# Kernel optimization log

Hardware: AMD Instinct MI355X
Metric: run time of the kernel (lower is better)

The kernel has to match this reference:

```python
import jax, jax.numpy as jnp
import numpy as np

B, H, W, D = 16, 14, 14, 512   # map_dim D == attention_dim A (required by broadcast add)
L, HID, A = 32, 512, 512


def setup_inputs() -> dict:
    key = jax.random.key(0)
    ks = jax.random.split(key, 8)
    s = 0.02
    return {
        "maps": jax.random.normal(ks[0], (B, H, W, D), jnp.float32),
        "hiddens": jax.random.normal(ks[1], (B, L, HID), jnp.float32),
        "W_hidden": jax.random.normal(ks[2], (A, HID), jnp.float32) * s,
        "b_hidden": jnp.zeros((A,), jnp.float32),
        "W_rect": jax.random.normal(ks[3], (1, A), jnp.float32) * s,
        "b_rect": jnp.zeros((1,), jnp.float32),
        "W_co": jax.random.normal(ks[4], (HID, D), jnp.float32) * s,
        "b_co": jnp.zeros((HID,), jnp.float32),
    }


def reference(maps, hiddens, W_hidden, b_hidden, W_rect, b_rect, W_co, b_co):
    b, h, w, d = maps.shape
    fmaps = maps.reshape(b, h * w, d)                       # (B, P, D)
    hlin = hiddens @ W_hidden.T + b_hidden                  # (B, L, A)
    # additive co-attention score: ReLU(fmaps + hlin) -> linear to scalar
    rect = jax.nn.relu(fmaps[:, None, :, :] + hlin[:, :, None, :])  # (B, L, P, A)
    scores = jnp.einsum('blpa,a->blp', rect, W_rect[0]) + b_rect[0]  # (B, L, P)
    attn = jax.nn.softmax(scores, axis=2)                   # softmax over pixels P
    ctx = jnp.einsum('blp,bpd->bld', attn, fmaps)           # (B, L, D)
    co_att = (ctx @ W_co.T + b_co) * hiddens                # (B, L, HID)
    return co_att, attn
```

## Files before the change

### kernel.cpp

```cpp
#include <hip/hip_runtime.h>
#include <math.h>


typedef __attribute__((ext_vector_type(8))) short short8;
typedef __attribute__((ext_vector_type(4))) float f32x4;

__device__ __forceinline__ unsigned f2bf_u(float x) {
    union { float f; unsigned u; } c; c.f = x;
    return (c.u + 0x7FFFu + ((c.u >> 16) & 1u)) >> 16;
}
__device__ __forceinline__ unsigned pack2(float lo, float hi) {
    return f2bf_u(lo) | (f2bf_u(hi) << 16);
}
__device__ __forceinline__ uint4 pack8(const float4 a, const float4 b) {
    uint4 r;
    r.x = pack2(a.x, a.y); r.y = pack2(a.z, a.w);
    r.z = pack2(b.x, b.y); r.w = pack2(b.z, b.w);
    return r;
}

__device__ __forceinline__ void wait16(int* flags, int base) {
    if (threadIdx.x < 16) {
        while (__hip_atomic_fetch_add(&flags[(base + threadIdx.x) * 16], 0,
                                      __ATOMIC_RELAXED, __HIP_MEMORY_SCOPE_AGENT) < 1)
            __builtin_amdgcn_s_sleep(8);
    }
    __syncthreads();
    __builtin_amdgcn_fence(__ATOMIC_ACQUIRE, "agent");
}

__device__ __forceinline__ void signal1(int* flags, int idx) {
    __syncthreads();
    if (threadIdx.x == 0)
        __hip_atomic_store(&flags[idx * 16], 1, __ATOMIC_RELEASE, __HIP_MEMORY_SCOPE_AGENT);
}

template<int MODE>
__device__ __forceinline__ void gemm_body(
    const float* __restrict__ Af, const unsigned short* __restrict__ Ab,
    const float* __restrict__ Bf, const float* __restrict__ bias,
    const float* __restrict__ hmul, float* __restrict__ C,
    char* smem, int m0, int n0)
{
    uint4* As = (uint4*)smem;
    uint4* Bs = (uint4*)(smem + 32768);
    float* red = (float*)smem;
    const int tid = threadIdx.x;

    #pragma unroll
    for (int j = 0; j < 8; ++j) {
        const int S = tid + 256 * j;
        const int i = S >> 6, ln = S & 63;
        const int row  = (i & 1) * 16 + (ln & 15);
        const int col8 = (i >> 1) * 4 + (ln >> 4);
        uint4 av;
        if (MODE == 0) {
            const float* ap = Af + (size_t)(m0 + row) * 512 + col8 * 8;
            av = pack8(*(const float4*)ap, *(const float4*)(ap + 4));
        } else {
            av = *(const uint4*)(Ab + (size_t)(m0 + row) * 512 + col8 * 8);
        }
        const float* bp = Bf + (size_t)(n0 + row) * 512 + col8 * 8;
        As[S] = av;
        Bs[S] = pack8(*(const float4*)bp, *(const float4*)(bp + 4));
    }
    __syncthreads();

    const int w = tid >> 6, ln = tid & 63;
    f32x4 acc[4];
    #pragma unroll
    for (int fo = 0; fo < 4; ++fo) acc[fo] = (f32x4){0.f,0.f,0.f,0.f};
    #pragma unroll
    for (int sl = 0; sl < 4; ++sl) {
        const int s = 4 * w + sl;
        const short8 a0 = *(const short8*)&As[(2*s+0)*64 + ln];
        const short8 a1 = *(const short8*)&As[(2*s+1)*64 + ln];
        const short8 b0 = *(const short8*)&Bs[(2*s+0)*64 + ln];
        const short8 b1 = *(const short8*)&Bs[(2*s+1)*64 + ln];
        acc[0] = __builtin_amdgcn_mfma_f32_16x16x32_bf16(a0, b0, acc[0], 0, 0, 0);
        acc[1] = __builtin_amdgcn_mfma_f32_16x16x32_bf16(a0, b1, acc[1], 0, 0, 0);
        acc[2] = __builtin_amdgcn_mfma_f32_16x16x32_bf16(a1, b0, acc[2], 0, 0, 0);
        acc[3] = __builtin_amdgcn_mfma_f32_16x16x32_bf16(a1, b1, acc[3], 0, 0, 0);
    }
    __syncthreads();
    #pragma unroll
    for (int fo = 0; fo < 4; ++fo)
        #pragma unroll
        for (int r = 0; r < 4; ++r)
            red[w*1024 + fo*256 + r*64 + ln] = acc[fo][r];
    __syncthreads();
    #pragma unroll
    for (int j = 0; j < 4; ++j) {
        const int o = tid + 256 * j;
        float v = red[o] + red[1024 + o] + red[2048 + o] + red[3072 + o];
        const int fo = o >> 8, r = (o >> 6) & 3, l2 = o & 63;
        const int m = m0 + (fo >> 1) * 16 + ((l2 >> 4) << 2) + r;
        const int n = n0 + (fo & 1) * 16 + (l2 & 15);
        v += bias[n];
        if (MODE == 1) v *= hmul[(size_t)m * 512 + n];
        C[(size_t)m * 512 + n] = v;
    }
}

__device__ __forceinline__ void mid_body(
    const float* __restrict__ maps, const float* __restrict__ hlin,
    const float* __restrict__ W_rect, const float* __restrict__ b_rect,
    float* __restrict__ attn_out, unsigned int* __restrict__ ctx_out,
    char* smem, int b, int s)
{
    float* h0    = (float*)smem;
    float* h1    = h0 + 512;
    float* wv    = h0 + 1024;
    float* ftile = h0 + 1536;
    float* sraw  = ftile + 16 * 516;
    float* ep    = sraw + 2 * 208;
    float* bc    = ep + 32;

    const int l0 = 2 * s;
    const int tid = threadIdx.x;
    const int pi = tid >> 4, k = tid & 15;

    {
        const float4* H0 = (const float4*)(hlin + ((size_t)b * 32 + l0) * 512);
        const float4* H1 = (const float4*)(hlin + ((size_t)b * 32 + l0 + 1) * 512);
        const float4* WV = (const float4*)W_rect;
        if (tid < 128) { ((float4*)h0)[tid] = H0[tid]; ((float4*)wv)[tid] = WV[tid]; }
        else           { ((float4*)h1)[tid - 128] = H1[tid - 128]; }
    }
    __syncthreads();

    int aoff[8];
    float4 h0r[8], h1r[8], wr[8];
    #pragma unroll
    for (int j = 0; j < 8; ++j) {
        aoff[j] = k * 32 + ((j + k) & 7) * 4;
        h0r[j] = *(const float4*)&h0[aoff[j]];
        h1r[j] = *(const float4*)&h1[aoff[j]];
        wr[j]  = *(const float4*)&wv[aoff[j]];
    }

    const float* mb = maps + (size_t)b * 196 * 512;
    const float br = b_rect[0];
    const int d0 = tid * 2;

    float m0 = -INFINITY, m1 = -INFINITY, ls0 = 0.f, ls1 = 0.f;
    float cA0 = 0.f, cA1 = 0.f, cB0 = 0.f, cB1 = 0.f;

    for (int c = 0; c < 13; ++c) {
        __syncthreads();
        #pragma unroll
        for (int it = 0; it < 8; ++it) {
            const int idx = tid + 256 * it;
            const int r = idx >> 7, c4 = idx & 127;
            int p = c * 16 + r; if (p > 195) p = 195;
            *(float4*)&ftile[r * 516 + c4 * 4] = *(const float4*)(mb + (size_t)p * 512 + c4 * 4);
        }
        __syncthreads();

        float s0 = 0.f, s1 = 0.f;
        #pragma unroll
        for (int j = 0; j < 8; ++j) {
            const float4 f = *(const float4*)&ftile[pi * 516 + aoff[j]];
            const float4 A = h0r[j], Bv = h1r[j], W = wr[j];
            s0 += fmaxf(f.x + A.x, 0.f) * W.x + fmaxf(f.y + A.y, 0.f) * W.y
                + fmaxf(f.z + A.z, 0.f) * W.z + fmaxf(f.w + A.w, 0.f) * W.w;
            s1 += fmaxf(f.x + Bv.x, 0.f) * W.x + fmaxf(f.y + Bv.y, 0.f) * W.y
                + fmaxf(f.z + Bv.z, 0.f) * W.z + fmaxf(f.w + Bv.w, 0.f) * W.w;
        }
        #pragma unroll
        for (int msk = 1; msk <= 8; msk <<= 1) {
            s0 += __shfl_xor(s0, msk);
            s1 += __shfl_xor(s1, msk);
        }
        if (k == 0) {
            const int p = c * 16 + pi;
            const bool ok = (p <= 195);
            sraw[p]       = ok ? (s0 + br) : -INFINITY;
            sraw[208 + p] = ok ? (s1 + br) : -INFINITY;
        }
        __syncthreads();

        if (tid < 32) {
            const int l = tid >> 4, pl = tid & 15;
            const float sc = sraw[l * 208 + c * 16 + pl];
            float mx = sc;
            #pragma unroll
            for (int msk = 1; msk <= 8; msk <<= 1) mx = fmaxf(mx, __shfl_xor(mx, msk));
            const float nm = fmaxf(l ? m1 : m0, mx);
            const float e = (sc == -INFINITY) ? 0.f : __expf(sc - nm);
            ep[l * 16 + pl] = e;
            float es = e;
            #pragma unroll
            for (int msk = 1; msk <= 8; msk <<= 1) es += __shfl_xor(es, msk);
            if (pl == 0) { bc[l] = mx; bc[2 + l] = es; }
        }
        __syncthreads();

        const float nm0 = fmaxf(m0, bc[0]), nm1 = fmaxf(m1, bc[1]);
        const float al0 = __expf(m0 - nm0), al1 = __expf(m1 - nm1);
        ls0 = ls0 * al0 + bc[2];
        ls1 = ls1 * al1 + bc[3];
        m0 = nm0; m1 = nm1;
        cA0 *= al0; cA1 *= al0; cB0 *= al1; cB1 *= al1;
        #pragma unroll
        for (int r = 0; r < 16; ++r) {
            const float2 f = *(const float2*)&ftile[r * 516 + d0];
            const float w0 = ep[r], w1 = ep[16 + r];
            cA0 += w0 * f.x; cA1 += w0 * f.y;
            cB0 += w1 * f.x; cB1 += w1 * f.y;
        }
    }

    const float inv0 = 1.f / ls0, inv1 = 1.f / ls1;
    ctx_out[((size_t)b * 32 + l0) * 256 + tid]     = pack2(cA0 * inv0, cA1 * inv0);
    ctx_out[((size_t)b * 32 + l0 + 1) * 256 + tid] = pack2(cB0 * inv1, cB1 * inv1);
    for (int idx = tid; idx < 392; idx += 256) {
        const int l = idx & 1, p = idx >> 1;
        const float sc = sraw[l * 208 + p];
        attn_out[((size_t)b * 32 + l0 + l) * 196 + p] =
            __expf(sc - (l ? m1 : m0)) * (l ? inv1 : inv0);
    }
}

__global__ __launch_bounds__(256) void coatt_combo_kernel(
    const float* __restrict__ maps, const float* __restrict__ hiddens,
    const float* __restrict__ W_hidden, const float* __restrict__ b_hidden,
    const float* __restrict__ W_rect, const float* __restrict__ b_rect,
    const float* __restrict__ W_co, const float* __restrict__ b_co,
    float* __restrict__ out_co, float* __restrict__ out_attn,
    unsigned int* __restrict__ ctx32, int* __restrict__ flag1,
    int* __restrict__ flag2)
{
    __shared__ __align__(16) char smem[65536];
    const int bx = blockIdx.x;

    if (bx < 256) {
        gemm_body<0>(hiddens, (const unsigned short*)nullptr, W_hidden, b_hidden,
                     (const float*)nullptr, out_co, smem,
                     (bx >> 4) * 32, (bx & 15) * 32);
        signal1(flag1, bx);
    } else if (bx < 512) {
        const int bid2 = bx - 256, b = bid2 >> 4, s = bid2 & 15;
        wait16(flag1, b * 16);
        mid_body(maps, out_co, W_rect, b_rect, out_attn, ctx32, smem, b, s);
        signal1(flag2, bid2);
    } else {
        const int bid2 = bx - 512, b = bid2 >> 4;
        wait16(flag2, b * 16);
        gemm_body<1>((const float*)nullptr, (const unsigned short*)ctx32, W_co,
                     b_co, hiddens, out_co, smem,
                     (bid2 >> 4) * 32, (bid2 & 15) * 32);
    }
}

extern "C" void kernel_launch(void* const* d_in, const int* in_sizes, int n_in,
                              void* d_out, int out_size, void* d_ws, size_t ws_size,
                              hipStream_t stream)
{
    const float* maps     = (const float*)d_in[0];
    const float* hiddens  = (const float*)d_in[1];
    const float* W_hidden = (const float*)d_in[2];
    const float* b_hidden = (const float*)d_in[3];
    const float* W_rect   = (const float*)d_in[4];
    const float* b_rect   = (const float*)d_in[5];
    const float* W_co     = (const float*)d_in[6];
    const float* b_co     = (const float*)d_in[7];

    float* out_co   = (float*)d_out;
    float* out_attn = out_co + (size_t)512 * 512;

    char* ws = (char*)d_ws;
    unsigned int* ctx32 = (unsigned int*)ws;
    int* flag1 = (int*)(ws + (1 << 20));
    int* flag2 = (int*)(ws + (1 << 20) + (64 << 10));

    hipLaunchKernelGGL(coatt_combo_kernel, dim3(768), dim3(256), 0, stream,
                       maps, hiddens, W_hidden, b_hidden, W_rect, b_rect,
                       W_co, b_co, out_co, out_attn, ctx32, flag1, flag2);
}
```

Baseline: 127.7 us.

## Fuse all stages into one per-block kernel with FP32 GEMV projections

Replaces the three-role flag-synchronised kernel (bf16 MFMA GEMM, attention, bf16 MFMA GEMM) with one 256-block kernel. Each block computes its own two rows of the hidden projection and output projection as FP32 GEMVs, which removes the inter-block atomic flags, spin-waits and workspace round trips. In exchange every block re-reads the full W_hidden and W_co (1 MB each) from cache. It also drops tensor-core use and runs more scalar FP32 math per block. Precision improves because bf16 rounding is gone.

```diff
diff --git a/kernel.cpp b/kernel.cpp
--- a/kernel.cpp
+++ b/kernel.cpp
@@ -2,254 +2,196 @@
 #include <math.h>
 
 
-typedef __attribute__((ext_vector_type(8))) short short8;
-typedef __attribute__((ext_vector_type(4))) float f32x4;
-
-__device__ __forceinline__ unsigned f2bf_u(float x) {
-    union { float f; unsigned u; } c; c.f = x;
-    return (c.u + 0x7FFFu + ((c.u >> 16) & 1u)) >> 16;
-}
-__device__ __forceinline__ unsigned pack2(float lo, float hi) {
-    return f2bf_u(lo) | (f2bf_u(hi) << 16);
-}
-__device__ __forceinline__ uint4 pack8(const float4 a, const float4 b) {
-    uint4 r;
-    r.x = pack2(a.x, a.y); r.y = pack2(a.z, a.w);
-    r.z = pack2(b.x, b.y); r.w = pack2(b.z, b.w);
-    return r;
-}
-
-__device__ __forceinline__ void wait16(int* flags, int base) {
-    if (threadIdx.x < 16) {
-        while (__hip_atomic_fetch_add(&flags[(base + threadIdx.x) * 16], 0,
-                                      __ATOMIC_RELAXED, __HIP_MEMORY_SCOPE_AGENT) < 1)
-            __builtin_amdgcn_s_sleep(8);
-    }
-    __syncthreads();
-    __builtin_amdgcn_fence(__ATOMIC_ACQUIRE, "agent");
-}
-
-__device__ __forceinline__ void signal1(int* flags, int idx) {
-    __syncthreads();
-    if (threadIdx.x == 0)
-        __hip_atomic_store(&flags[idx * 16], 1, __ATOMIC_RELEASE, __HIP_MEMORY_SCOPE_AGENT);
-}
-
-template<int MODE>
-__device__ __forceinline__ void gemm_body(
-    const float* __restrict__ Af, const unsigned short* __restrict__ Ab,
-    const float* __restrict__ Bf, const float* __restrict__ bias,
-    const float* __restrict__ hmul, float* __restrict__ C,
-    char* smem, int m0, int n0)
-{
-    uint4* As = (uint4*)smem;
-    uint4* Bs = (uint4*)(smem + 32768);
-    float* red = (float*)smem;
-    const int tid = threadIdx.x;
-
-    #pragma unroll
-    for (int j = 0; j < 8; ++j) {
-        const int S = tid + 256 * j;
-        const int i = S >> 6, ln = S & 63;
-        const int row  = (i & 1) * 16 + (ln & 15);
-        const int col8 = (i >> 1) * 4 + (ln >> 4);
-        uint4 av;
-        if (MODE == 0) {
-            const float* ap = Af + (size_t)(m0 + row) * 512 + col8 * 8;
-            av = pack8(*(const float4*)ap, *(const float4*)(ap + 4));
-        } else {
-            av = *(const uint4*)(Ab + (size_t)(m0 + row) * 512 + col8 * 8);
-        }
-        const float* bp = Bf + (size_t)(n0 + row) * 512 + col8 * 8;
-        As[S] = av;
-        Bs[S] = pack8(*(const float4*)bp, *(const float4*)(bp + 4));
-    }
-    __syncthreads();
-
-    const int w = tid >> 6, ln = tid & 63;
-    f32x4 acc[4];
-    #pragma unroll
-    for (int fo = 0; fo < 4; ++fo) acc[fo] = (f32x4){0.f,0.f,0.f,0.f};
-    #pragma unroll
-    for (int sl = 0; sl < 4; ++sl) {
-        const int s = 4 * w + sl;
-        const short8 a0 = *(const short8*)&As[(2*s+0)*64 + ln];
-        const short8 a1 = *(const short8*)&As[(2*s+1)*64 + ln];
-        const short8 b0 = *(const short8*)&Bs[(2*s+0)*64 + ln];
-        const short8 b1 = *(const short8*)&Bs[(2*s+1)*64 + ln];
-        acc[0] = __builtin_amdgcn_mfma_f32_16x16x32_bf16(a0, b0, acc[0], 0, 0, 0);
-        acc[1] = __builtin_amdgcn_mfma_f32_16x16x32_bf16(a0, b1, acc[1], 0, 0, 0);
-        acc[2] = __builtin_amdgcn_mfma_f32_16x16x32_bf16(a1, b0, acc[2], 0, 0, 0);
-        acc[3] = __builtin_amdgcn_mfma_f32_16x16x32_bf16(a1, b1, acc[3], 0, 0, 0);
-    }
-    __syncthreads();
-    #pragma unroll
-    for (int fo = 0; fo < 4; ++fo)
-        #pragma unroll
-        for (int r = 0; r < 4; ++r)
-            red[w*1024 + fo*256 + r*64 + ln] = acc[fo][r];
-    __syncthreads();
-    #pragma unroll
-    for (int j = 0; j < 4; ++j) {
-        const int o = tid + 256 * j;
-        float v = red[o] + red[1024 + o] + red[2048 + o] + red[3072 + o];
-        const int fo = o >> 8, r = (o >> 6) & 3, l2 = o & 63;
-        const int m = m0 + (fo >> 1) * 16 + ((l2 >> 4) << 2) + r;
-        const int n = n0 + (fo & 1) * 16 + (l2 & 15);
-        v += bias[n];
-        if (MODE == 1) v *= hmul[(size_t)m * 512 + n];
-        C[(size_t)m * 512 + n] = v;
-    }
-}
-
-__device__ __forceinline__ void mid_body(
-    const float* __restrict__ maps, const float* __restrict__ hlin,
-    const float* __restrict__ W_rect, const float* __restrict__ b_rect,
-    float* __restrict__ attn_out, unsigned int* __restrict__ ctx_out,
-    char* smem, int b, int s)
-{
-    float* h0    = (float*)smem;
-    float* h1    = h0 + 512;
-    float* wv    = h0 + 1024;
-    float* ftile = h0 + 1536;
-    float* sraw  = ftile + 16 * 516;
-    float* ep    = sraw + 2 * 208;
-    float* bc    = ep + 32;
-
-    const int l0 = 2 * s;
-    const int tid = threadIdx.x;
-    const int pi = tid >> 4, k = tid & 15;
-
-    {
-        const float4* H0 = (const float4*)(hlin + ((size_t)b * 32 + l0) * 512);
-        const float4* H1 = (const float4*)(hlin + ((size_t)b * 32 + l0 + 1) * 512);
-        const float4* WV = (const float4*)W_rect;
-        if (tid < 128) { ((float4*)h0)[tid] = H0[tid]; ((float4*)wv)[tid] = WV[tid]; }
-        else           { ((float4*)h1)[tid - 128] = H1[tid - 128]; }
-    }
-    __syncthreads();
-
-    int aoff[8];
-    float4 h0r[8], h1r[8], wr[8];
-    #pragma unroll
-    for (int j = 0; j < 8; ++j) {
-        aoff[j] = k * 32 + ((j + k) & 7) * 4;
-        h0r[j] = *(const float4*)&h0[aoff[j]];
-        h1r[j] = *(const float4*)&h1[aoff[j]];
-        wr[j]  = *(const float4*)&wv[aoff[j]];
-    }
-
-    const float* mb = maps + (size_t)b * 196 * 512;
-    const float br = b_rect[0];
-    const int d0 = tid * 2;
-
-    float m0 = -INFINITY, m1 = -INFINITY, ls0 = 0.f, ls1 = 0.f;
-    float cA0 = 0.f, cA1 = 0.f, cB0 = 0.f, cB1 = 0.f;
-
-    for (int c = 0; c < 13; ++c) {
-        __syncthreads();
-        #pragma unroll
-        for (int it = 0; it < 8; ++it) {
-            const int idx = tid + 256 * it;
-            const int r = idx >> 7, c4 = idx & 127;
-            int p = c * 16 + r; if (p > 195) p = 195;
-            *(float4*)&ftile[r * 516 + c4 * 4] = *(const float4*)(mb + (size_t)p * 512 + c4 * 4);
-        }
-        __syncthreads();
-
-        float s0 = 0.f, s1 = 0.f;
-        #pragma unroll
-        for (int j = 0; j < 8; ++j) {
-            const float4 f = *(const float4*)&ftile[pi * 516 + aoff[j]];
-            const float4 A = h0r[j], Bv = h1r[j], W = wr[j];
-            s0 += fmaxf(f.x + A.x, 0.f) * W.x + fmaxf(f.y + A.y, 0.f) * W.y
-                + fmaxf(f.z + A.z, 0.f) * W.z + fmaxf(f.w + A.w, 0.f) * W.w;
-            s1 += fmaxf(f.x + Bv.x, 0.f) * W.x + fmaxf(f.y + Bv.y, 0.f) * W.y
-                + fmaxf(f.z + Bv.z, 0.f) * W.z + fmaxf(f.w + Bv.w, 0.f) * W.w;
-        }
-        #pragma unroll
-        for (int msk = 1; msk <= 8; msk <<= 1) {
-            s0 += __shfl_xor(s0, msk);
-            s1 += __shfl_xor(s1, msk);
-        }
-        if (k == 0) {
-            const int p = c * 16 + pi;
-            const bool ok = (p <= 195);
-            sraw[p]       = ok ? (s0 + br) : -INFINITY;
-            sraw[208 + p] = ok ? (s1 + br) : -INFINITY;
-        }
-        __syncthreads();
-
-        if (tid < 32) {
-            const int l = tid >> 4, pl = tid & 15;
-            const float sc = sraw[l * 208 + c * 16 + pl];
-            float mx = sc;
-            #pragma unroll
-            for (int msk = 1; msk <= 8; msk <<= 1) mx = fmaxf(mx, __shfl_xor(mx, msk));
-            const float nm = fmaxf(l ? m1 : m0, mx);
-            const float e = (sc == -INFINITY) ? 0.f : __expf(sc - nm);
-            ep[l * 16 + pl] = e;
-            float es = e;
-            #pragma unroll
-            for (int msk = 1; msk <= 8; msk <<= 1) es += __shfl_xor(es, msk);
-            if (pl == 0) { bc[l] = mx; bc[2 + l] = es; }
-        }
-        __syncthreads();
-
-        const float nm0 = fmaxf(m0, bc[0]), nm1 = fmaxf(m1, bc[1]);
-        const float al0 = __expf(m0 - nm0), al1 = __expf(m1 - nm1);
-        ls0 = ls0 * al0 + bc[2];
-        ls1 = ls1 * al1 + bc[3];
-        m0 = nm0; m1 = nm1;
-        cA0 *= al0; cA1 *= al0; cB0 *= al1; cB1 *= al1;
-        #pragma unroll
-        for (int r = 0; r < 16; ++r) {
-            const float2 f = *(const float2*)&ftile[r * 516 + d0];
-            const float w0 = ep[r], w1 = ep[16 + r];
-            cA0 += w0 * f.x; cA1 += w0 * f.y;
-            cB0 += w1 * f.x; cB1 += w1 * f.y;
-        }
-    }
-
-    const float inv0 = 1.f / ls0, inv1 = 1.f / ls1;
-    ctx_out[((size_t)b * 32 + l0) * 256 + tid]     = pack2(cA0 * inv0, cA1 * inv0);
-    ctx_out[((size_t)b * 32 + l0 + 1) * 256 + tid] = pack2(cB0 * inv1, cB1 * inv1);
-    for (int idx = tid; idx < 392; idx += 256) {
-        const int l = idx & 1, p = idx >> 1;
-        const float sc = sraw[l * 208 + p];
-        attn_out[((size_t)b * 32 + l0 + l) * 196 + p] =
-            __expf(sc - (l ? m1 : m0)) * (l ? inv1 : inv0);
-    }
-}
-
-__global__ __launch_bounds__(256) void coatt_combo_kernel(
+__global__ __launch_bounds__(256) void coatt_onekernel(
     const float* __restrict__ maps, const float* __restrict__ hiddens,
     const float* __restrict__ W_hidden, const float* __restrict__ b_hidden,
     const float* __restrict__ W_rect, const float* __restrict__ b_rect,
     const float* __restrict__ W_co, const float* __restrict__ b_co,
-    float* __restrict__ out_co, float* __restrict__ out_attn,
-    unsigned int* __restrict__ ctx32, int* __restrict__ flag1,
-    int* __restrict__ flag2)
+    float* __restrict__ out_co, float* __restrict__ out_attn)
 {
-    __shared__ __align__(16) char smem[65536];
-    const int bx = blockIdx.x;
-
-    if (bx < 256) {
-        gemm_body<0>(hiddens, (const unsigned short*)nullptr, W_hidden, b_hidden,
-                     (const float*)nullptr, out_co, smem,
-                     (bx >> 4) * 32, (bx & 15) * 32);
-        signal1(flag1, bx);
-    } else if (bx < 512) {
-        const int bid2 = bx - 256, b = bid2 >> 4, s = bid2 & 15;
-        wait16(flag1, b * 16);
-        mid_body(maps, out_co, W_rect, b_rect, out_attn, ctx32, smem, b, s);
-        signal1(flag2, bid2);
-    } else {
-        const int bid2 = bx - 512, b = bid2 >> 4;
-        wait16(flag2, b * 16);
-        gemm_body<1>((const float*)nullptr, (const unsigned short*)ctx32, W_co,
-                     b_co, hiddens, out_co, smem,
-                     (bid2 >> 4) * 32, (bid2 & 15) * 32);
+    __shared__ float hid0[512], hid1[512], wv[512];
+    __shared__ float hl0[512], hl1[512];
+    __shared__ float ctx0[512], ctx1[512];
+    __shared__ float ftile[16 * 516];
+    __shared__ float sraw[2 * 208];
+    __shared__ float ep[32];
+    __shared__ float bc[4];
+
+    const int b = blockIdx.x >> 4, s = blockIdx.x & 15;
+    const int l0 = 2 * s;
+    const int tid = threadIdx.x;
+    const int kc = tid & 15, aslot = tid >> 4;
+
+    {
+        const float4* H0 = (const float4*)(hiddens + ((size_t)b * 32 + l0) * 512);
+        const float4* H1 = (const float4*)(hiddens + ((size_t)b * 32 + l0 + 1) * 512);
+        const float4* WV = (const float4*)W_rect;
+        if (tid < 128) { ((float4*)hid0)[tid] = H0[tid]; ((float4*)wv)[tid] = WV[tid]; }
+        else           { ((float4*)hid1)[tid - 128] = H1[tid - 128]; }
+    }
+    __syncthreads();
+
+    int koff[8];
+    #pragma unroll
+    for (int j = 0; j < 8; ++j) koff[j] = kc * 32 + ((j + kc) & 7) * 4;
+
+    {
+        float4 hA[8], hB[8];
+        #pragma unroll
+        for (int j = 0; j < 8; ++j) {
+            hA[j] = *(const float4*)&hid0[koff[j]];
+            hB[j] = *(const float4*)&hid1[koff[j]];
+        }
+        for (int it = 0; it < 32; ++it) {
+            const int a = it * 16 + aslot;
+            const float* wrow = W_hidden + (size_t)a * 512;
+            float a0 = 0.f, a1 = 0.f;
+            #pragma unroll
+            for (int j = 0; j < 8; ++j) {
+                const float4 w = *(const float4*)(wrow + koff[j]);
+                a0 += w.x*hA[j].x + w.y*hA[j].y + w.z*hA[j].z + w.w*hA[j].w;
+                a1 += w.x*hB[j].x + w.y*hB[j].y + w.z*hB[j].z + w.w*hB[j].w;
+            }
+            #pragma unroll
+            for (int msk = 1; msk <= 8; msk <<= 1) {
+                a0 += __shfl_xor(a0, msk);
+                a1 += __shfl_xor(a1, msk);
+            }
+            if (kc == 0) {
+                const float bh = b_hidden[a];
+                hl0[a] = a0 + bh;
+                hl1[a] = a1 + bh;
+            }
+        }
+    }
+    __syncthreads();
+
+    {
+        const int pi = tid >> 4, k = kc;
+        int aoff[8];
+        float4 h0r[8], h1r[8], wr[8];
+        #pragma unroll
+        for (int j = 0; j < 8; ++j) {
+            aoff[j] = koff[j];
+            h0r[j] = *(const float4*)&hl0[aoff[j]];
+            h1r[j] = *(const float4*)&hl1[aoff[j]];
+            wr[j]  = *(const float4*)&wv[aoff[j]];
+        }
+        const float* mb = maps + (size_t)b * 196 * 512;
+        const float br = b_rect[0];
+        const int d0 = tid * 2;
+
+        float m0 = -INFINITY, m1 = -INFINITY, ls0 = 0.f, ls1 = 0.f;
+        float cA0 = 0.f, cA1 = 0.f, cB0 = 0.f, cB1 = 0.f;
+
+        for (int c = 0; c < 13; ++c) {
+            __syncthreads();
+            #pragma unroll
+            for (int it = 0; it < 8; ++it) {
+                const int idx = tid + 256 * it;
+                const int r = idx >> 7, c4 = idx & 127;
+                int p = c * 16 + r; if (p > 195) p = 195;
+                *(float4*)&ftile[r * 516 + c4 * 4] =
+                    *(const float4*)(mb + (size_t)p * 512 + c4 * 4);
+            }
+            __syncthreads();
+
+            float s0 = 0.f, s1 = 0.f;
+            #pragma unroll
+            for (int j = 0; j < 8; ++j) {
+                const float4 f = *(const float4*)&ftile[pi * 516 + aoff[j]];
+                const float4 A = h0r[j], Bv = h1r[j], W = wr[j];
+                s0 += fmaxf(f.x + A.x, 0.f) * W.x + fmaxf(f.y + A.y, 0.f) * W.y
+                    + fmaxf(f.z + A.z, 0.f) * W.z + fmaxf(f.w + A.w, 0.f) * W.w;
+                s1 += fmaxf(f.x + Bv.x, 0.f) * W.x + fmaxf(f.y + Bv.y, 0.f) * W.y
+                    + fmaxf(f.z + Bv.z, 0.f) * W.z + fmaxf(f.w + Bv.w, 0.f) * W.w;
+            }
+            #pragma unroll
+            for (int msk = 1; msk <= 8; msk <<= 1) {
+                s0 += __shfl_xor(s0, msk);
+                s1 += __shfl_xor(s1, msk);
+            }
+            if (k == 0) {
+                const int p = c * 16 + pi;
+                const bool ok = (p <= 195);
+                sraw[p]       = ok ? (s0 + br) : -INFINITY;
+                sraw[208 + p] = ok ? (s1 + br) : -INFINITY;
+            }
+            __syncthreads();
+
+            if (tid < 32) {
+                const int l = tid >> 4, pl = tid & 15;
+                const float sc = sraw[l * 208 + c * 16 + pl];
+                float mx = sc;
+                #pragma unroll
+                for (int msk = 1; msk <= 8; msk <<= 1) mx = fmaxf(mx, __shfl_xor(mx, msk));
+                const float nm = fmaxf(l ? m1 : m0, mx);
+                const float e = (sc == -INFINITY) ? 0.f : __expf(sc - nm);
+                ep[l * 16 + pl] = e;
+                float es = e;
+                #pragma unroll
+                for (int msk = 1; msk <= 8; msk <<= 1) es += __shfl_xor(es, msk);
+                if (pl == 0) { bc[l] = mx; bc[2 + l] = es; }
+            }
+            __syncthreads();
+
+            const float nm0 = fmaxf(m0, bc[0]), nm1 = fmaxf(m1, bc[1]);
+            const float al0 = __expf(m0 - nm0), al1 = __expf(m1 - nm1);
+            ls0 = ls0 * al0 + bc[2];
+            ls1 = ls1 * al1 + bc[3];
+            m0 = nm0; m1 = nm1;
+            cA0 *= al0; cA1 *= al0; cB0 *= al1; cB1 *= al1;
+            #pragma unroll
+            for (int r = 0; r < 16; ++r) {
+                const float2 f = *(const float2*)&ftile[r * 516 + d0];
+                const float w0 = ep[r], w1 = ep[16 + r];
+                cA0 += w0 * f.x; cA1 += w0 * f.y;
+                cB0 += w1 * f.x; cB1 += w1 * f.y;
+            }
+        }
+
+        const float inv0 = 1.f / ls0, inv1 = 1.f / ls1;
+        ctx0[d0] = cA0 * inv0; ctx0[d0 + 1] = cA1 * inv0;
+        ctx1[d0] = cB0 * inv1; ctx1[d0 + 1] = cB1 * inv1;
+        for (int idx = tid; idx < 392; idx += 256) {
+            const int l = idx & 1, p = idx >> 1;
+            const float sc = sraw[l * 208 + p];
+            out_attn[((size_t)b * 32 + l0 + l) * 196 + p] =
+                __expf(sc - (l ? m1 : m0)) * (l ? inv1 : inv0);
+        }
+    }
+    __syncthreads();
+
+    {
+        float4 xA[8], xB[8];
+        #pragma unroll
+        for (int j = 0; j < 8; ++j) {
+            xA[j] = *(const float4*)&ctx0[koff[j]];
+            xB[j] = *(const float4*)&ctx1[koff[j]];
+        }
+        float* o0 = out_co + ((size_t)b * 32 + l0) * 512;
+        float* o1 = o0 + 512;
+        for (int it = 0; it < 32; ++it) {
+            const int h = it * 16 + aslot;
+            const float* wrow = W_co + (size_t)h * 512;
+            float a0 = 0.f, a1 = 0.f;
+            #pragma unroll
+            for (int j = 0; j < 8; ++j) {
+                const float4 w = *(const float4*)(wrow + koff[j]);
+                a0 += w.x*xA[j].x + w.y*xA[j].y + w.z*xA[j].z + w.w*xA[j].w;
+                a1 += w.x*xB[j].x + w.y*xB[j].y + w.z*xB[j].z + w.w*xB[j].w;
+            }
+            #pragma unroll
+            for (int msk = 1; msk <= 8; msk <<= 1) {
+                a0 += __shfl_xor(a0, msk);
+                a1 += __shfl_xor(a1, msk);
+            }
+            if (kc == 0) {
+                const float bo = b_co[h];
+                o0[h] = (a0 + bo) * hid0[h];
+                o1[h] = (a1 + bo) * hid1[h];
+            }
+        }
     }
 }
 
@@ -269,12 +211,7 @@
     float* out_co   = (float*)d_out;
     float* out_attn = out_co + (size_t)512 * 512;
 
-    char* ws = (char*)d_ws;
-    unsigned int* ctx32 = (unsigned int*)ws;
-    int* flag1 = (int*)(ws + (1 << 20));
-    int* flag2 = (int*)(ws + (1 << 20) + (64 << 10));
-
-    hipLaunchKernelGGL(coatt_combo_kernel, dim3(768), dim3(256), 0, stream,
+    hipLaunchKernelGGL(coatt_onekernel, dim3(256), dim3(256), 0, stream,
                        maps, hiddens, W_hidden, b_hidden, W_rect, b_rect,
-                       W_co, b_co, out_co, out_attn, ctx32, flag1, flag2);
+                       W_co, b_co, out_co, out_attn);
 }
```

New measurement: 150.9 us. +18.1%, slower.
